# Optimization experiments

Measured on AMD Instinct MI355X. Metric: run time of the kernel, lower is better.

## Reference

```python
import jax, jax.numpy as jnp
import numpy as np

B, ZD, E, L, NL = 64, 512, 512, 8192, 1000


def irm(x, Ws, bs):
    # IRMLinear(d, n_layers=2): stack of residual linear blocks x <- x + Linear(x)
    for W, b in zip(Ws, bs):
        x = x + x @ W.T + b
    return x


def setup_inputs() -> dict:
    key = jax.random.key(0)
    ks = jax.random.split(key, 10)
    s = lambda k, sh: (jax.random.normal(k, sh, jnp.float32) * 0.02)
    return dict(
        z=jax.random.normal(ks[0], (B, ZD), jnp.float32),
        y=jax.random.randint(ks[1], (B,), 0, NL),
        W_yemb=s(ks[2], (E, NL)), b_yemb=jnp.zeros((E,), jnp.float32),
        Wy1=s(ks[3], (E, E)), by1=jnp.zeros((E,), jnp.float32),
        Wy2=s(ks[4], (E, E)), by2=jnp.zeros((E,), jnp.float32),
        Wz1=s(ks[5], (ZD, ZD)), bz1=jnp.zeros((ZD,), jnp.float32),
        Wz2=s(ks[6], (ZD, ZD)), bz2=jnp.zeros((ZD,), jnp.float32),
        W_zlat=s(ks[7], (L, ZD)),          # Linear(z_dim, lat_size, bias=False)
        w_proj=s(ks[8], (E,)),             # Linear(embed_size, 1, bias=False)
    )


def reference(z, y, W_yemb, b_yemb, Wy1, by1, Wy2, by2, Wz1, bz1, Wz2, bz2, W_zlat, w_proj):
    # y: int64 class ids -> one-hot via identity embedding_mat
    yembed = jax.nn.one_hot(y, NL, dtype=jnp.float32)            # [B, NL]
    ye = yembed @ W_yemb.T + b_yemb                               # [B, E]
    ye = irm(ye, [Wy1, Wy2], [by1, by2])                          # [B, E]
    zz = irm(z, [Wz1, Wz2], [bz1, bz2])                           # [B, ZD]
    zl = zz @ W_zlat.T                                            # [B, L]
    # bmm(z[:,:,1], ye[:,1,:]) then lat_proj over embed collapses to a
    # per-batch scalar: lat[b,i] = zl[b,i] * (ye[b] . w_proj)  (same math,
    # avoids the [B, L, E] intermediate)
    s_scal = ye @ w_proj                                          # [B]
    return zl * s_scal[:, None]                                   # [B, L]
```

## Files before the change

### kernel.cpp

```cpp
#include <hip/hip_runtime.h>


#define BB 64
#define DD 512
#define LL 8192
#define NLBL 1000
#define PIT 68

typedef __attribute__((ext_vector_type(8))) short short8;
typedef __attribute__((ext_vector_type(4))) float f32x4;

__device__ __forceinline__ unsigned short f2bf(float f) {
  unsigned u = __float_as_uint(f);
  return (unsigned short)((u + 0x7fffu + ((u >> 16) & 1u)) >> 16);
}

__device__ __forceinline__ void matvec_block(int eblk, const float* __restrict__ W,
                                             const float* __restrict__ vin,
                                             float* __restrict__ vout) {
  __shared__ float vl[DD];
  __shared__ float red[256];
  int tid = threadIdx.x;
  vl[tid] = vin[tid];
  vl[tid + 256] = vin[tid + 256];
  __syncthreads();
  int el = tid & 31, jg = tid >> 5;
  int e = eblk * 32 + el;
  float acc = 0.f;
  for (int j = jg; j < DD; j += 8)
    acc += W[j * DD + e] * vl[j];
  red[tid] = acc;
  __syncthreads();
  if (tid < 32) {
    float s = vl[eblk * 32 + tid];
#pragma unroll
    for (int g = 0; g < 8; ++g) s += red[g * 32 + tid];
    vout[eblk * 32 + tid] = s;
  }
}

template <int FIRST>
__device__ __forceinline__ void layer_gemm(int blk, const float* __restrict__ Xg,
                                           const float* __restrict__ Pin,
                                           const float* __restrict__ W,
                                           const float* __restrict__ bias,
                                           float* __restrict__ P) {
  __shared__ __align__(16) float Xs[BB][PIT];
  __shared__ __align__(16) float Ws[32][PIT];
  int tid = threadIdx.x;
  int jt = blk >> 3, ks = blk & 7;
  int j0 = jt * 32, k0 = ks * 64;
#pragma unroll
  for (int i = 0; i < 4; ++i) {
    int slot = tid + i * 256, row = slot >> 4, c4 = (slot & 15) * 4;
    float4 v;
    if (FIRST) {
      v = *(const float4*)&Xg[row * DD + k0 + c4];
    } else {
      v = float4{0.f, 0.f, 0.f, 0.f};
#pragma unroll
      for (int s = 0; s < 8; ++s) {
        float4 p = *(const float4*)&Pin[(s * BB + row) * DD + k0 + c4];
        v.x += p.x; v.y += p.y; v.z += p.z; v.w += p.w;
      }
    }
    *(float4*)&Xs[row][c4] = v;
  }
#pragma unroll
  for (int i = 0; i < 2; ++i) {
    int slot = tid + i * 256, row = slot >> 4, c4 = (slot & 15) * 4;
    *(float4*)&Ws[row][c4] = *(const float4*)&W[(j0 + row) * DD + k0 + c4];
  }
  __syncthreads();
  int jl = tid & 15, bl = tid >> 4;
  float acc[4][2] = {};
#pragma unroll
  for (int k = 0; k < 64; k += 4) {
    float4 xv[4], wv[2];
#pragma unroll
    for (int i = 0; i < 4; ++i) xv[i] = *(const float4*)&Xs[bl + 16 * i][k];
#pragma unroll
    for (int u = 0; u < 2; ++u) wv[u] = *(const float4*)&Ws[jl + 16 * u][k];
#pragma unroll
    for (int i = 0; i < 4; ++i)
#pragma unroll
      for (int u = 0; u < 2; ++u)
        acc[i][u] += xv[i].x * wv[u].x + xv[i].y * wv[u].y +
                     xv[i].z * wv[u].z + xv[i].w * wv[u].w;
  }
#pragma unroll
  for (int i = 0; i < 4; ++i) {
    int b = bl + 16 * i;
#pragma unroll
    for (int u = 0; u < 2; ++u) {
      int jj = j0 + jl + 16 * u;
      float v = acc[i][u];
      if (ks == 0) {
        float xr;
        if (FIRST) {
          xr = Xg[b * DD + jj];
        } else {
          xr = 0.f;
#pragma unroll
          for (int s = 0; s < 8; ++s) xr += Pin[(s * BB + b) * DD + jj];
        }
        v += xr + bias[jj];
      }
      P[(ks * BB + b) * DD + jj] = v;
    }
  }
}

__global__ __launch_bounds__(256) void kA(const float* __restrict__ z,
                                          const float* __restrict__ Wz1,
                                          const float* __restrict__ bz1,
                                          float* __restrict__ P1,
                                          const float* __restrict__ Wy2,
                                          const float* __restrict__ w_proj,
                                          float* __restrict__ u1) {
  int blk = blockIdx.x;
  if (blk < 128) layer_gemm<1>(blk, z, nullptr, Wz1, bz1, P1);
  else           matvec_block(blk - 128, Wy2, w_proj, u1);
}

__global__ __launch_bounds__(256) void kB(const float* __restrict__ P1,
                                          const float* __restrict__ Wz2,
                                          const float* __restrict__ bz2,
                                          float* __restrict__ P2,
                                          const float* __restrict__ Wy1,
                                          const float* __restrict__ u1,
                                          float* __restrict__ u0,
                                          const float* __restrict__ by1,
                                          const float* __restrict__ by2,
                                          const float* __restrict__ w_proj,
                                          float* __restrict__ d2) {
  int blk = blockIdx.x;
  if (blk < 128) {
    layer_gemm<0>(blk, nullptr, P1, Wz2, bz2, P2);
  } else if (blk < 144) {
    matvec_block(blk - 128, Wy1, u1, u0);
  } else {
    __shared__ float red[256];
    int tid = threadIdx.x;
    float p = by1[tid] * u1[tid] + by2[tid] * w_proj[tid] +
              by1[tid + 256] * u1[tid + 256] + by2[tid + 256] * w_proj[tid + 256];
    red[tid] = p;
    __syncthreads();
    if (tid < 64) {
      float s = red[tid] + red[tid + 64] + red[tid + 128] + red[tid + 192];
#pragma unroll
      for (int d = 32; d; d >>= 1) s += __shfl_down(s, d, 64);
      if (tid == 0) d2[0] = s;
    }
  }
}

__global__ __launch_bounds__(256) void kZ(const float* __restrict__ P2,
                                          unsigned short* __restrict__ zzs,
                                          const float* __restrict__ W_yemb,
                                          const float* __restrict__ b_yemb,
                                          const int* __restrict__ y,
                                          const float* __restrict__ u0,
                                          const float* __restrict__ d2) {
  __shared__ float s4[4];
  int cid = blockIdx.x, tid = threadIdx.x;
  int bloc = tid >> 6, lane = tid & 63;
  int bb = cid * 4 + bloc;
  int yb = y[bb];
  int e0 = lane * 8;
  float4 ua = *(const float4*)&u0[e0];
  float4 ub = *(const float4*)&u0[e0 + 4];
  float4 ba = *(const float4*)&b_yemb[e0];
  float4 bb4 = *(const float4*)&b_yemb[e0 + 4];
  const float* wy = W_yemb + yb;
  float sg = (wy[(size_t)(e0 + 0) * NLBL] + ba.x) * ua.x +
             (wy[(size_t)(e0 + 1) * NLBL] + ba.y) * ua.y +
             (wy[(size_t)(e0 + 2) * NLBL] + ba.z) * ua.z +
             (wy[(size_t)(e0 + 3) * NLBL] + ba.w) * ua.w +
             (wy[(size_t)(e0 + 4) * NLBL] + bb4.x) * ub.x +
             (wy[(size_t)(e0 + 5) * NLBL] + bb4.y) * ub.y +
             (wy[(size_t)(e0 + 6) * NLBL] + bb4.z) * ub.z +
             (wy[(size_t)(e0 + 7) * NLBL] + bb4.w) * ub.w;
#pragma unroll
  for (int d = 32; d; d >>= 1) sg += __shfl_down(sg, d, 64);
  if (lane == 0) s4[bloc] = sg + d2[0];
  __syncthreads();
  float sv = s4[bloc];
  int eo = cid * 2048 + tid * 8;
  float4 a0 = {0.f, 0.f, 0.f, 0.f}, a1 = {0.f, 0.f, 0.f, 0.f};
#pragma unroll
  for (int s = 0; s < 8; ++s) {
    const float* p = P2 + s * (BB * DD) + eo;
    float4 x = *(const float4*)p;
    float4 q = *(const float4*)(p + 4);
    a0.x += x.x; a0.y += x.y; a0.z += x.z; a0.w += x.w;
    a1.x += q.x; a1.y += q.y; a1.z += q.z; a1.w += q.w;
  }
  short8 h = {(short)f2bf(a0.x * sv), (short)f2bf(a0.y * sv),
              (short)f2bf(a0.z * sv), (short)f2bf(a0.w * sv),
              (short)f2bf(a1.x * sv), (short)f2bf(a1.y * sv),
              (short)f2bf(a1.z * sv), (short)f2bf(a1.w * sv)};
  *(short8*)&zzs[eo] = h;
}

__global__ __launch_bounds__(256) void kC(const unsigned short* __restrict__ zzs,
                                          const float* __restrict__ W,
                                          float* __restrict__ out) {
  __shared__ __align__(16) unsigned short Bs[16 * 512];
  int tid = threadIdx.x;
  int l0 = blockIdx.x * 16;
#pragma unroll
  for (int i = 0; i < 4; ++i) {
    int gi = tid + i * 256, row = gi >> 6, c = gi & 63;
    const float* src = &W[(size_t)(l0 + row) * DD + c * 8];
    float4 v0 = *(const float4*)src;
    float4 v1 = *(const float4*)(src + 4);
    short8 h = {(short)f2bf(v0.x), (short)f2bf(v0.y), (short)f2bf(v0.z),
                (short)f2bf(v0.w), (short)f2bf(v1.x), (short)f2bf(v1.y),
                (short)f2bf(v1.z), (short)f2bf(v1.w)};
    *(short8*)&Bs[row * DD + ((c ^ (row & 7)) << 3)] = h;
  }
  __syncthreads();
  int wave = tid >> 6, lane = tid & 63, quad = lane >> 4, l15 = lane & 15;
  const unsigned short* arow = zzs + (wave * 16 + l15) * DD + quad * 8;
  f32x4 acc = {};
  short8 apf[4];
#pragma unroll
  for (int p = 0; p < 4; ++p) apf[p] = *(const short8*)(arow + p * 32);
#pragma unroll
  for (int kc = 0; kc < 4; ++kc) {
    short8 cur[4] = {apf[0], apf[1], apf[2], apf[3]};
    if (kc < 3) {
#pragma unroll
      for (int p = 0; p < 4; ++p)
        apf[p] = *(const short8*)(arow + (kc + 1) * 128 + p * 32);
    }
#pragma unroll
    for (int s = 0; s < 4; ++s) {
      int c = kc * 16 + s * 4 + quad;
      short8 bf = *(const short8*)&Bs[l15 * DD + ((c ^ (l15 & 7)) << 3)];
      acc = __builtin_amdgcn_mfma_f32_16x16x32_bf16(cur[s], bf, acc, 0, 0, 0);
    }
  }
#pragma unroll
  for (int reg = 0; reg < 4; ++reg) {
    int b = wave * 16 + quad * 4 + reg;
    out[(size_t)b * LL + l0 + l15] = acc[reg];
  }
}

extern "C" void kernel_launch(void* const* d_in, const int* in_sizes, int n_in,
                              void* d_out, int out_size, void* d_ws, size_t ws_size,
                              hipStream_t stream) {
  const float* z      = (const float*)d_in[0];
  const int*   y      = (const int*)  d_in[1];
  const float* W_yemb = (const float*)d_in[2];
  const float* b_yemb = (const float*)d_in[3];
  const float* Wy1    = (const float*)d_in[4];
  const float* by1    = (const float*)d_in[5];
  const float* Wy2    = (const float*)d_in[6];
  const float* by2    = (const float*)d_in[7];
  const float* Wz1    = (const float*)d_in[8];
  const float* bz1    = (const float*)d_in[9];
  const float* Wz2    = (const float*)d_in[10];
  const float* bz2    = (const float*)d_in[11];
  const float* W_zlat = (const float*)d_in[12];
  const float* w_proj = (const float*)d_in[13];

  float* ws = (float*)d_ws;
  float* P1 = ws;
  float* P2 = ws + 262144;
  unsigned short* zzs = (unsigned short*)(ws + 524288);
  float* u1 = ws + 540672;
  float* u0 = ws + 541184;
  float* d2 = ws + 541696;
  float* out = (float*)d_out;

  kA<<<144, 256, 0, stream>>>(z, Wz1, bz1, P1, Wy2, w_proj, u1);
  kB<<<145, 256, 0, stream>>>(P1, Wz2, bz2, P2, Wy1, u1, u0, by1, by2, w_proj, d2);
  kZ<<<16, 256, 0, stream>>>(P2, zzs, W_yemb, b_yemb, y, u0, d2);
  kC<<<512, 256, 0, stream>>>(zzs, W_zlat, out);
}
```

Measured before the change: 142.9 us.

## Replace split-K layer GEMMs with full-K GEMMs and fold scalar into final GEMM

The two residual-layer GEMMs now run over the full K dimension per block instead of writing split-K partials that a later kernel had to sum. This removes the separate reduction kernel kZ and the large partial-sum buffers. The y-embedding path now computes the gathered embedding times Wy1 directly, as a GEMM run alongside the first layer. The per-batch scalar is applied in the epilogue of the final MFMA GEMM rather than before bf16 conversion. The launch count drops from four to three, but each GEMM block now reads full weight rows from global memory without an LDS tile and does more serial work per thread.

```diff
diff --git a/kernel.cpp b/kernel.cpp
--- a/kernel.cpp
+++ b/kernel.cpp
@@ -5,7 +5,6 @@
 #define DD 512
 #define LL 8192
 #define NLBL 1000
-#define PIT 68
 
 typedef __attribute__((ext_vector_type(8))) short short8;
 typedef __attribute__((ext_vector_type(4))) float f32x4;
@@ -39,176 +38,134 @@
   }
 }
 
-template <int FIRST>
-__device__ __forceinline__ void layer_gemm(int blk, const float* __restrict__ Xg,
-                                           const float* __restrict__ Pin,
-                                           const float* __restrict__ W,
-                                           const float* __restrict__ bias,
-                                           float* __restrict__ P) {
-  __shared__ __align__(16) float Xs[BB][PIT];
-  __shared__ __align__(16) float Ws[32][PIT];
-  int tid = threadIdx.x;
-  int jt = blk >> 3, ks = blk & 7;
-  int j0 = jt * 32, k0 = ks * 64;
-#pragma unroll
-  for (int i = 0; i < 4; ++i) {
-    int slot = tid + i * 256, row = slot >> 4, c4 = (slot & 15) * 4;
-    float4 v;
-    if (FIRST) {
-      v = *(const float4*)&Xg[row * DD + k0 + c4];
-    } else {
-      v = float4{0.f, 0.f, 0.f, 0.f};
-#pragma unroll
-      for (int s = 0; s < 8; ++s) {
-        float4 p = *(const float4*)&Pin[(s * BB + row) * DD + k0 + c4];
-        v.x += p.x; v.y += p.y; v.z += p.z; v.w += p.w;
-      }
-    }
-    *(float4*)&Xs[row][c4] = v;
-  }
-#pragma unroll
-  for (int i = 0; i < 2; ++i) {
-    int slot = tid + i * 256, row = slot >> 4, c4 = (slot & 15) * 4;
-    *(float4*)&Ws[row][c4] = *(const float4*)&W[(j0 + row) * DD + k0 + c4];
-  }
-  __syncthreads();
-  int jl = tid & 15, bl = tid >> 4;
-  float acc[4][2] = {};
-#pragma unroll
-  for (int k = 0; k < 64; k += 4) {
-    float4 xv[4], wv[2];
-#pragma unroll
-    for (int i = 0; i < 4; ++i) xv[i] = *(const float4*)&Xs[bl + 16 * i][k];
-#pragma unroll
-    for (int u = 0; u < 2; ++u) wv[u] = *(const float4*)&Ws[jl + 16 * u][k];
-#pragma unroll
-    for (int i = 0; i < 4; ++i)
-#pragma unroll
-      for (int u = 0; u < 2; ++u)
-        acc[i][u] += xv[i].x * wv[u].x + xv[i].y * wv[u].y +
-                     xv[i].z * wv[u].z + xv[i].w * wv[u].w;
-  }
-#pragma unroll
-  for (int i = 0; i < 4; ++i) {
-    int b = bl + 16 * i;
-#pragma unroll
-    for (int u = 0; u < 2; ++u) {
-      int jj = j0 + jl + 16 * u;
-      float v = acc[i][u];
-      if (ks == 0) {
-        float xr;
-        if (FIRST) {
-          xr = Xg[b * DD + jj];
-        } else {
-          xr = 0.f;
-#pragma unroll
-          for (int s = 0; s < 8; ++s) xr += Pin[(s * BB + b) * DD + jj];
-        }
-        v += xr + bias[jj];
-      }
-      P[(ks * BB + b) * DD + jj] = v;
-    }
-  }
-}
-
-__global__ __launch_bounds__(256) void kA(const float* __restrict__ z,
-                                          const float* __restrict__ Wz1,
-                                          const float* __restrict__ bz1,
-                                          float* __restrict__ P1,
-                                          const float* __restrict__ Wy2,
-                                          const float* __restrict__ w_proj,
-                                          float* __restrict__ u1) {
+template <int GATHER, int BF16OUT, int JW, int HASBIAS>
+__device__ __forceinline__ void gemm_fullk(
+    int blk, const float* __restrict__ Ain,
+    const float* __restrict__ Wemb, const float* __restrict__ bemb,
+    const int* __restrict__ y,
+    const float* __restrict__ W, const float* __restrict__ bias,
+    float* __restrict__ outf, unsigned short* __restrict__ outh) {
+  __shared__ __align__(16) float As[8][DD];
+  int tid = threadIdx.x;
+  constexpr int NJT = DD / JW;
+  int bt = blk / NJT, jt = blk % NJT;
+  int b0 = bt * 8, j0 = jt * JW;
+  if (GATHER) {
+#pragma unroll
+    for (int r = 0; r < 8; ++r) {
+      int yb = y[b0 + r];
+      As[r][tid]       = Wemb[(size_t)tid * NLBL + yb]         + bemb[tid];
+      As[r][tid + 256] = Wemb[(size_t)(tid + 256) * NLBL + yb] + bemb[tid + 256];
+    }
+  } else {
+#pragma unroll
+    for (int i = 0; i < 4; ++i) {
+      int g = tid + i * 256;
+      int row = g >> 7, c4 = (g & 127) << 2;
+      *(float4*)&As[row][c4] = *(const float4*)&Ain[(size_t)(b0 + row) * DD + c4];
+    }
+  }
+  __syncthreads();
+  int jl = tid & 31, bg = tid >> 5;
+  constexpr int NO = JW / 32;
+  const float* wr[NO];
+#pragma unroll
+  for (int o = 0; o < NO; ++o) wr[o] = W + (size_t)(j0 + o * 32 + jl) * DD;
+  float a0[NO] = {}, a1[NO] = {}, a2[NO] = {}, a3[NO] = {};
+#pragma unroll 4
+  for (int k4 = 0; k4 < 128; ++k4) {
+    float4 av = *(const float4*)&As[bg][k4 << 2];
+#pragma unroll
+    for (int o = 0; o < NO; ++o) {
+      float4 wv = *(const float4*)&wr[o][k4 << 2];
+      a0[o] = fmaf(av.x, wv.x, a0[o]);
+      a1[o] = fmaf(av.y, wv.y, a1[o]);
+      a2[o] = fmaf(av.z, wv.z, a2[o]);
+      a3[o] = fmaf(av.w, wv.w, a3[o]);
+    }
+  }
+#pragma unroll
+  for (int o = 0; o < NO; ++o) {
+    int j = j0 + o * 32 + jl;
+    float v = (a0[o] + a1[o]) + (a2[o] + a3[o]) + As[bg][j];
+    if (HASBIAS) v += bias[j];
+    if (BF16OUT) outh[(size_t)(b0 + bg) * DD + j] = f2bf(v);
+    else         outf[(size_t)(b0 + bg) * DD + j] = v;
+  }
+}
+
+__device__ __forceinline__ void s_block(int cid, const float* __restrict__ GH,
+                                        const float* __restrict__ u1,
+                                        const float* __restrict__ by1,
+                                        const float* __restrict__ by2,
+                                        const float* __restrict__ w_proj,
+                                        float* __restrict__ sv) {
+  __shared__ float red[256];
+  __shared__ float d2s;
+  int tid = threadIdx.x;
+  float p = by1[tid] * u1[tid] + by2[tid] * w_proj[tid] +
+            by1[tid + 256] * u1[tid + 256] + by2[tid + 256] * w_proj[tid + 256];
+  red[tid] = p;
+  __syncthreads();
+  if (tid < 64) {
+    float s = red[tid] + red[tid + 64] + red[tid + 128] + red[tid + 192];
+#pragma unroll
+    for (int d = 32; d; d >>= 1) s += __shfl_down(s, d, 64);
+    if (tid == 0) d2s = s;
+  }
+  __syncthreads();
+  int bloc = tid >> 6, lane = tid & 63;
+  int b = cid * 4 + bloc;
+  int e0 = lane * 8;
+  float4 g0 = *(const float4*)&GH[(size_t)b * DD + e0];
+  float4 g1 = *(const float4*)&GH[(size_t)b * DD + e0 + 4];
+  float4 ua = *(const float4*)&u1[e0];
+  float4 ub = *(const float4*)&u1[e0 + 4];
+  float sg = g0.x * ua.x + g0.y * ua.y + g0.z * ua.z + g0.w * ua.w +
+             g1.x * ub.x + g1.y * ub.y + g1.z * ub.z + g1.w * ub.w;
+#pragma unroll
+  for (int d = 32; d; d >>= 1) sg += __shfl_down(sg, d, 64);
+  if (lane == 0) sv[b] = sg + d2s;
+}
+
+__global__ __launch_bounds__(256) void k1(
+    const float* __restrict__ z, const float* __restrict__ Wz1,
+    const float* __restrict__ bz1, float* __restrict__ X1,
+    const float* __restrict__ Wy2, const float* __restrict__ w_proj,
+    float* __restrict__ u1, const float* __restrict__ W_yemb,
+    const float* __restrict__ b_yemb, const int* __restrict__ y,
+    const float* __restrict__ Wy1, float* __restrict__ GH) {
   int blk = blockIdx.x;
-  if (blk < 128) layer_gemm<1>(blk, z, nullptr, Wz1, bz1, P1);
-  else           matvec_block(blk - 128, Wy2, w_proj, u1);
-}
-
-__global__ __launch_bounds__(256) void kB(const float* __restrict__ P1,
-                                          const float* __restrict__ Wz2,
-                                          const float* __restrict__ bz2,
-                                          float* __restrict__ P2,
-                                          const float* __restrict__ Wy1,
-                                          const float* __restrict__ u1,
-                                          float* __restrict__ u0,
-                                          const float* __restrict__ by1,
-                                          const float* __restrict__ by2,
-                                          const float* __restrict__ w_proj,
-                                          float* __restrict__ d2) {
+  if (blk < 64)
+    gemm_fullk<1, 0, 64, 0>(blk, nullptr, W_yemb, b_yemb, y, Wy1, nullptr, GH, nullptr);
+  else if (blk < 192)
+    gemm_fullk<0, 0, 32, 1>(blk - 64, z, nullptr, nullptr, nullptr, Wz1, bz1, X1, nullptr);
+  else
+    matvec_block(blk - 192, Wy2, w_proj, u1);
+}
+
+__global__ __launch_bounds__(256) void k2(
+    const float* __restrict__ X1, const float* __restrict__ Wz2,
+    const float* __restrict__ bz2, unsigned short* __restrict__ zzs,
+    const float* __restrict__ GH, const float* __restrict__ u1,
+    const float* __restrict__ by1, const float* __restrict__ by2,
+    const float* __restrict__ w_proj, float* __restrict__ sv) {
   int blk = blockIdx.x;
-  if (blk < 128) {
-    layer_gemm<0>(blk, nullptr, P1, Wz2, bz2, P2);
-  } else if (blk < 144) {
-    matvec_block(blk - 128, Wy1, u1, u0);
-  } else {
-    __shared__ float red[256];
-    int tid = threadIdx.x;
-    float p = by1[tid] * u1[tid] + by2[tid] * w_proj[tid] +
-              by1[tid + 256] * u1[tid + 256] + by2[tid + 256] * w_proj[tid + 256];
-    red[tid] = p;
-    __syncthreads();
-    if (tid < 64) {
-      float s = red[tid] + red[tid + 64] + red[tid + 128] + red[tid + 192];
-#pragma unroll
-      for (int d = 32; d; d >>= 1) s += __shfl_down(s, d, 64);
-      if (tid == 0) d2[0] = s;
-    }
-  }
-}
-
-__global__ __launch_bounds__(256) void kZ(const float* __restrict__ P2,
-                                          unsigned short* __restrict__ zzs,
-                                          const float* __restrict__ W_yemb,
-                                          const float* __restrict__ b_yemb,
-                                          const int* __restrict__ y,
-                                          const float* __restrict__ u0,
-                                          const float* __restrict__ d2) {
-  __shared__ float s4[4];
-  int cid = blockIdx.x, tid = threadIdx.x;
-  int bloc = tid >> 6, lane = tid & 63;
-  int bb = cid * 4 + bloc;
-  int yb = y[bb];
-  int e0 = lane * 8;
-  float4 ua = *(const float4*)&u0[e0];
-  float4 ub = *(const float4*)&u0[e0 + 4];
-  float4 ba = *(const float4*)&b_yemb[e0];
-  float4 bb4 = *(const float4*)&b_yemb[e0 + 4];
-  const float* wy = W_yemb + yb;
-  float sg = (wy[(size_t)(e0 + 0) * NLBL] + ba.x) * ua.x +
-             (wy[(size_t)(e0 + 1) * NLBL] + ba.y) * ua.y +
-             (wy[(size_t)(e0 + 2) * NLBL] + ba.z) * ua.z +
-             (wy[(size_t)(e0 + 3) * NLBL] + ba.w) * ua.w +
-             (wy[(size_t)(e0 + 4) * NLBL] + bb4.x) * ub.x +
-             (wy[(size_t)(e0 + 5) * NLBL] + bb4.y) * ub.y +
-             (wy[(size_t)(e0 + 6) * NLBL] + bb4.z) * ub.z +
-             (wy[(size_t)(e0 + 7) * NLBL] + bb4.w) * ub.w;
-#pragma unroll
-  for (int d = 32; d; d >>= 1) sg += __shfl_down(sg, d, 64);
-  if (lane == 0) s4[bloc] = sg + d2[0];
-  __syncthreads();
-  float sv = s4[bloc];
-  int eo = cid * 2048 + tid * 8;
-  float4 a0 = {0.f, 0.f, 0.f, 0.f}, a1 = {0.f, 0.f, 0.f, 0.f};
-#pragma unroll
-  for (int s = 0; s < 8; ++s) {
-    const float* p = P2 + s * (BB * DD) + eo;
-    float4 x = *(const float4*)p;
-    float4 q = *(const float4*)(p + 4);
-    a0.x += x.x; a0.y += x.y; a0.z += x.z; a0.w += x.w;
-    a1.x += q.x; a1.y += q.y; a1.z += q.z; a1.w += q.w;
-  }
-  short8 h = {(short)f2bf(a0.x * sv), (short)f2bf(a0.y * sv),
-              (short)f2bf(a0.z * sv), (short)f2bf(a0.w * sv),
-              (short)f2bf(a1.x * sv), (short)f2bf(a1.y * sv),
-              (short)f2bf(a1.z * sv), (short)f2bf(a1.w * sv)};
-  *(short8*)&zzs[eo] = h;
+  if (blk < 128)
+    gemm_fullk<0, 1, 32, 1>(blk, X1, nullptr, nullptr, nullptr, Wz2, bz2, nullptr, zzs);
+  else
+    s_block(blk - 128, GH, u1, by1, by2, w_proj, sv);
 }
 
 __global__ __launch_bounds__(256) void kC(const unsigned short* __restrict__ zzs,
                                           const float* __restrict__ W,
+                                          const float* __restrict__ sv,
                                           float* __restrict__ out) {
   __shared__ __align__(16) unsigned short Bs[16 * 512];
+  __shared__ float ss[64];
   int tid = threadIdx.x;
   int l0 = blockIdx.x * 16;
+  if (tid < 64) ss[tid] = sv[tid];
 #pragma unroll
   for (int i = 0; i < 4; ++i) {
     int gi = tid + i * 256, row = gi >> 6, c = gi & 63;
@@ -245,7 +202,7 @@
 #pragma unroll
   for (int reg = 0; reg < 4; ++reg) {
     int b = wave * 16 + quad * 4 + reg;
-    out[(size_t)b * LL + l0 + l15] = acc[reg];
+    out[(size_t)b * LL + l0 + l15] = acc[reg] * ss[b];
   }
 }
 
@@ -268,16 +225,14 @@
   const float* w_proj = (const float*)d_in[13];
 
   float* ws = (float*)d_ws;
-  float* P1 = ws;
-  float* P2 = ws + 262144;
-  unsigned short* zzs = (unsigned short*)(ws + 524288);
-  float* u1 = ws + 540672;
-  float* u0 = ws + 541184;
-  float* d2 = ws + 541696;
+  float* X1 = ws;
+  float* GH = ws + 32768;
+  float* u1 = ws + 65536;
+  float* sv = ws + 66048;
+  unsigned short* zzs = (unsigned short*)(ws + 66112);
   float* out = (float*)d_out;
 
-  kA<<<144, 256, 0, stream>>>(z, Wz1, bz1, P1, Wy2, w_proj, u1);
-  kB<<<145, 256, 0, stream>>>(P1, Wz2, bz2, P2, Wy1, u1, u0, by1, by2, w_proj, d2);
-  kZ<<<16, 256, 0, stream>>>(P2, zzs, W_yemb, b_yemb, y, u0, d2);
-  kC<<<512, 256, 0, stream>>>(zzs, W_zlat, out);
-}
+  k1<<<208, 256, 0, stream>>>(z, Wz1, bz1, X1, Wy2, w_proj, u1, W_yemb, b_yemb, y, Wy1, GH);
+  k2<<<144, 256, 0, stream>>>(X1, Wz2, bz2, zzs, GH, u1, by1, by2, w_proj, sv);
+  kC<<<512, 256, 0, stream>>>(zzs, W_zlat, sv, out);
+}
```

Result: slower. 146.9 us (+2.8%).
